# Kernel tuning notes

Hardware: AMD Instinct MI355X
Metric: run time of the kernel (lower is better)

The kernel has to match this reference:

```python
import jax, jax.numpy as jnp
import numpy as np

N_NODES = 10000
N_EDGES = 160000
H = 4            # attention heads
HID = 128        # out_channels == gnn_hidden_dim
C = HID          # per-head channels after .view(-1, H, C) with C = out_channels
HC = H * C       # 512
QD, KD, VD = 19, 16, 18
OUT = 2
SCALE = (HID // H) ** -0.5  # (out_channels // heads) ** -0.5


def _segment_softmax(alpha, idx, n):
    # PyG-style softmax over edges grouped by destination node, per head.
    amax = jax.ops.segment_max(alpha, idx, num_segments=n)          # [n, H]
    ex = jnp.exp(alpha - amax[idx])                                  # [E, H]
    den = jax.ops.segment_sum(ex, idx, num_segments=n)               # [n, H]
    return ex / (den[idx] + 1e-16)


def _gat_layer(qf, kf, vf, pos, src, dst, wq, wk, wv, wo, bo):
    n = qf.shape[0]
    q = (qf @ wq).reshape(n, H, C)
    k = (kf @ wk).reshape(n, H, C)
    v = (vf @ wv).reshape(n, H, C)
    # position-decayed attention: exp(-||pos_i - pos_j||), c_decay = 1.0
    dist = jnp.linalg.norm(pos[dst] - pos[src], axis=-1)             # [E]
    pos_weight = jnp.exp(-dist)
    alpha = (q[dst] * k[src]).sum(-1) * SCALE * pos_weight[:, None]  # [E, H]
    alpha = _segment_softmax(alpha, dst, n)
    out = jax.ops.segment_sum(v[src] * alpha[..., None], dst, num_segments=n)  # [n, H, C]
    return out.reshape(n, HC) @ wo + bo                              # concat heads -> lin_out


def setup_inputs() -> dict:
    key = jax.random.key(0)
    ks = jax.random.split(key, 16)

    def w(k, shape):  # xavier-uniform-ish scale
        return jax.random.normal(k, shape, jnp.float32) * np.float32(np.sqrt(2.0 / (shape[0] + shape[1])))

    obs = jax.random.normal(ks[0], (N_NODES, 37), jnp.float32)
    edge_index = jax.random.randint(ks[1], (2, N_EDGES), 0, N_NODES, jnp.int32)
    return dict(
        obs=obs, edge_index=edge_index,
        wq0=w(ks[2], (QD, HC)), wk0=w(ks[3], (KD, HC)), wv0=w(ks[4], (VD, HC)),
        wo0=w(ks[5], (HC, HID)), bo0=jnp.zeros((HID,), jnp.float32),
        wq1=w(ks[6], (HID, HC)), wk1=w(ks[7], (HID, HC)), wv1=w(ks[8], (HID, HC)),
        wo1=w(ks[9], (HC, HID)), bo1=jnp.zeros((HID,), jnp.float32),
        w1=w(ks[10], (HID, 256)), b1=jnp.zeros((256,), jnp.float32),
        w2=w(ks[11], (256, 256)), b2=jnp.zeros((256,), jnp.float32),
        w3=w(ks[12], (256, OUT)), b3=jnp.zeros((OUT,), jnp.float32),
    )


def reference(obs, edge_index, wq0, wk0, wv0, wo0, bo0, wq1, wk1, wv1, wo1, bo1, w1, b1, w2, b2, w3, b3):
    pos = obs[:, :2]
    # query: agent-self slices 0:12 plus tail slices 30:37 -> 19 dims
    qf = jnp.concatenate([obs[:, :12], obs[:, 30:37]], axis=-1)
    # key: neighbor_block 12:24 + obstacle_block 26:30 -> 16 dims
    kf = jnp.concatenate([obs[:, 12:24], obs[:, 26:30]], axis=-1)
    # value: neighbor_block + neighbor_progress + obstacle_block = 12:30 -> 18 dims
    vf = obs[:, 12:30]
    src, dst = edge_index[0], edge_index[1]
    h = _gat_layer(qf, kf, vf, pos, src, dst, wq0, wk0, wv0, wo0, bo0)
    h = _gat_layer(h, h, h, pos, src, dst, wq1, wk1, wv1, wo1, bo1)
    h = jax.nn.relu(h @ w1 + b1)
    h = jax.nn.relu(h @ w2 + b2)
    return h @ w3 + b3
```

## Files before the change

### kernel.cpp

```cpp
#include <hip/hip_runtime.h>
#include <math.h>

#define NN 10000
#define NE 160000
#define CAP 64
#define SCALE_F 0.17677669529663687f
#define LOG2E_F 1.4426950408889634f

typedef _Float16 f16x8 __attribute__((ext_vector_type(8)));
typedef _Float16 f16x2 __attribute__((ext_vector_type(2)));
typedef float f32x4 __attribute__((ext_vector_type(4)));

#if defined(__has_builtin)
#if __has_builtin(__builtin_amdgcn_global_load_lds)
#define HAS_GLL 1
#endif
#if __has_builtin(__builtin_amdgcn_fdot2)
#define HAS_FDOT2 1
#endif
#endif

struct __align__(8) Edge { int s; float pw; };

__device__ __forceinline__ float dot8_f16(f16x8 a, f16x8 b, float acc) {
#ifdef HAS_FDOT2
#pragma unroll
  for (int e = 0; e < 4; ++e) {
    f16x2 aa = {a[2 * e], a[2 * e + 1]};
    f16x2 bb = {b[2 * e], b[2 * e + 1]};
    acc = __builtin_amdgcn_fdot2(aa, bb, acc, false);
  }
#else
#pragma unroll
  for (int e = 0; e < 8; ++e) acc += (float)a[e] * (float)b[e];
#endif
  return acc;
}

__global__ __launch_bounds__(256) void scatter_kernel(const int* __restrict__ src, const int* __restrict__ dst,
                                                      const float* __restrict__ obs, int* __restrict__ counts,
                                                      Edge* __restrict__ edges) {
  int e = blockIdx.x * 256 + threadIdx.x;
  if (e >= NE) return;
  int s = src[e], d = dst[e];
  int p = atomicAdd(&counts[d], 1);
  float dx = obs[d * 37 + 0] - obs[s * 37 + 0];
  float dy = obs[d * 37 + 1] - obs[s * 37 + 1];
  Edge ee;
  ee.s = s;
  ee.pw = SCALE_F * LOG2E_F * __expf(-sqrtf(dx * dx + dy * dy));
  edges[d * CAP + p] = ee;
}

__global__ __launch_bounds__(256) void prep_kernel(const float* __restrict__ wq0, const float* __restrict__ wk0,
                                                   const float* __restrict__ wv0,
                                                   const float* __restrict__ wo0, const float* __restrict__ wq1,
                                                   const float* __restrict__ wk1, const float* __restrict__ wv1,
                                                   const float* __restrict__ wo1, const float* __restrict__ w1,
                                                   const float* __restrict__ w2, _Float16* __restrict__ dst,
                                                   const float* __restrict__ obs, _Float16* __restrict__ A0,
                                                   int* __restrict__ counts, const float* __restrict__ b3,
                                                   float* __restrict__ outg) {
  int t = blockIdx.x * 256 + threadIdx.x;
  if (t >= 524288) {
    int tp = t - 524288;
    if (tp < NN * 64) {
      int n = tp >> 6, k = tp & 63;
      const float* o = obs + n * 37;
      float x = 0.f;
      if (k < 12) x = o[k];
      else if (k < 19) x = o[30 + k - 12];
      else if (k < 31) x = o[12 + k - 19];
      else if (k < 35) x = o[26 + k - 31];
      else if (k < 53) x = o[12 + k - 35];
      A0[tp] = (_Float16)x;
      return;
    }
    int tz = tp - NN * 64;
    if (tz < NN) { counts[tz] = 0; return; }
    int to = tz - NN;
    if (to < 2 * NN) outg[to] = b3[to & 1];
    return;
  }
  if (t < 98304) {
    int c = t >> 6, k = t & 63;
    float x = 0.f;
    if (c < 512) { if (k < 19) x = wq0[k * 512 + c]; }
    else if (c < 1024) { if (k >= 19 && k < 35) x = wk0[(k - 19) * 512 + (c - 512)]; }
    else { if (k >= 35 && k < 53) x = wv0[(k - 35) * 512 + (c - 1024)]; }
    dst[t] = (_Float16)x;
    return;
  }
  int t1 = t - 98304;
  if (t1 < 196608) {
    int c = t1 >> 7, k = t1 & 127;
    float x;
    if (c < 512) x = wq1[k * 512 + c];
    else if (c < 1024) x = wk1[k * 512 + (c - 512)];
    else x = wv1[k * 512 + (c - 1024)];
    dst[98304 + t1] = (_Float16)x;
    return;
  }
  int t2 = t1 - 196608;
  if (t2 < 65536) { int n = t2 >> 9, k = t2 & 511; dst[294912 + t2] = (_Float16)wo0[k * 128 + n]; return; }
  int t3 = t2 - 65536;
  if (t3 < 65536) { int n = t3 >> 9, k = t3 & 511; dst[360448 + t3] = (_Float16)wo1[k * 128 + n]; return; }
  int t4 = t3 - 65536;
  if (t4 < 32768) { int n = t4 >> 7, k = t4 & 127; dst[425984 + t4] = (_Float16)w1[k * 256 + n]; return; }
  int t5 = t4 - 32768;
  if (t5 < 65536) { int n = t5 >> 8, k = t5 & 255; dst[458752 + t5] = (_Float16)w2[k * 256 + n]; }
}

__global__ __launch_bounds__(256) void gat_kernel(const _Float16* __restrict__ qh, const _Float16* __restrict__ KV,
                                                  const int* __restrict__ counts, const Edge* __restrict__ edges,
                                                  _Float16* __restrict__ attH) {
  int wave = threadIdx.x >> 6, lane = threadIdx.x & 63;
  int grp = lane >> 4, l15 = lane & 15;
  int r = blockIdx.x & 7;
  int c = blockIdx.x >> 3;
  int head = r & 3;
  int chunk = c * 2 + (r >> 2);
  int n = chunk * 4 + wave;
  const _Float16* kvbase = KV + (size_t)head * NN * 256 + l15 * 8;
  f16x8 qv = *(const f16x8*)(qh + (size_t)head * NN * 128 + n * 128 + l15 * 8);
  int cnt = counts[n];
  const Edge* eb = edges + (size_t)n * CAP;
  float den = 0.f;
  float o[8] = {};
  for (int j = grp; j < cnt; j += 8) {
    int jB = j + 4;
    bool actB = jB < cnt;
    int iB = actB ? jB : j;
    Edge eA = eb[j];
    Edge eB = eb[iB];
    const _Float16* pA = kvbase + (size_t)eA.s * 256;
    const _Float16* pB = kvbase + (size_t)eB.s * 256;
    f16x8 kA = *(const f16x8*)pA;
    f16x8 kB = *(const f16x8*)pB;
    f16x8 vA = *(const f16x8*)(pA + 128);
    f16x8 vB = *(const f16x8*)(pB + 128);
    float dA = dot8_f16(qv, kA, 0.f);
    float dB = dot8_f16(qv, kB, 0.f);
    dA += __shfl_xor(dA, 1); dB += __shfl_xor(dB, 1);
    dA += __shfl_xor(dA, 2); dB += __shfl_xor(dB, 2);
    dA += __shfl_xor(dA, 4); dB += __shfl_xor(dB, 4);
    dA += __shfl_xor(dA, 8); dB += __shfl_xor(dB, 8);
    float wA = exp2f(fminf(dA * eA.pw, 80.f));
    float wB = actB ? exp2f(fminf(dB * eB.pw, 80.f)) : 0.f;
    den += wA + wB;
#pragma unroll
    for (int e = 0; e < 8; ++e)
      o[e] += wA * (float)vA[e] + wB * (float)vB[e];
  }
#pragma unroll
  for (int off = 16; off <= 32; off <<= 1) {
    den += __shfl_xor(den, off);
#pragma unroll
    for (int e = 0; e < 8; ++e) o[e] += __shfl_xor(o[e], off);
  }
  if (grp == 0) {
    float inv = 1.f / (den + 1e-16f);
    f16x8 rr;
#pragma unroll
    for (int e = 0; e < 8; ++e) rr[e] = (_Float16)(o[e] * inv);
    *(f16x8*)(attH + (size_t)head * NN * 128 + n * 128 + l15 * 8) = rr;
  }
}

template <int BM, int BIAS, int RELU, int SPLIT, int FUSE3, int SEGA, int PIN>
__global__ __launch_bounds__(256) void gemm_mfma(const _Float16* __restrict__ A, const _Float16* __restrict__ BT,
                                                 const float* __restrict__ bias, _Float16* __restrict__ C,
                                                 _Float16* __restrict__ KV, const float* __restrict__ w3g,
                                                 float* __restrict__ outg, int M, int N, int K) {
  constexpr int ACH = BM / 32;
  constexpr int WR = BM / 2;
  constexpr int RF = WR / 16;
  __shared__ _Float16 As[2][BM * 64];
  __shared__ _Float16 Bs[2][64 * 64];
  int tid = threadIdx.x;
  int wave = tid >> 6, lane = tid & 63;
  int l15 = lane & 15, lq = lane >> 4;
  int wr = (wave >> 1) * WR, wc = (wave & 1) * 32;
  int bx, by;
  if (PIN) {
    int xcd = blockIdx.x & 7, slot = blockIdx.x >> 3;
    int hh = xcd & 3, half = xcd >> 2;
    int i = half * 237 + slot;
    int bg = i / 79;
    bx = i - bg * 79;
    by = (bg < 2) ? (2 * hh + bg) : (bg < 4) ? (8 + 2 * hh + (bg - 2)) : (16 + 2 * hh + (bg - 4));
  } else {
    bx = blockIdx.x;
    by = blockIdx.y;
  }
  int m0 = bx * BM, n0 = by * 64;
  f32x4 acc[RF][2] = {};
  int sw = (l15 & 7) << 4;
  int nt = K >> 6;

  auto stage = [&](int buf, int k0) {
#pragma unroll
    for (int i = 0; i < ACH; ++i) {
      int P = (wave * ACH + i) * 1024 + lane * 16;
      int row = P >> 7;
      int cl = (P & 127) ^ ((row & 7) << 4);
      int gr = m0 + row;
      if (gr > M - 1) gr = M - 1;
      const _Float16* g;
      if (SEGA)
        g = A + (size_t)(k0 >> 7) * (NN * 128) + (size_t)gr * 128 + (k0 & 64) + (cl >> 1);
      else
        g = A + (size_t)gr * K + k0 + (cl >> 1);
#ifdef HAS_GLL
      __builtin_amdgcn_global_load_lds((const __attribute__((address_space(1))) void*)g,
                                       (__attribute__((address_space(3))) void*)((char*)As[buf] + (wave * ACH + i) * 1024),
                                       16, 0, 0);
#else
      uint4 tv = *(const uint4*)g;
      *(uint4*)((char*)As[buf] + P) = tv;
#endif
    }
#pragma unroll
    for (int i = 0; i < 2; ++i) {
      int P = (wave * 2 + i) * 1024 + lane * 16;
      int row = P >> 7;
      int cl = (P & 127) ^ ((row & 7) << 4);
      const _Float16* g = BT + (size_t)(n0 + row) * K + k0 + (cl >> 1);
#ifdef HAS_GLL
      __builtin_amdgcn_global_load_lds((const __attribute__((address_space(1))) void*)g,
                                       (__attribute__((address_space(3))) void*)((char*)Bs[buf] + (wave * 2 + i) * 1024),
                                       16, 0, 0);
#else
      uint4 tv = *(const uint4*)g;
      *(uint4*)((char*)Bs[buf] + P) = tv;
#endif
    }
  };

  stage(0, 0);
  __syncthreads();
  for (int t = 0; t < nt; ++t) {
    int cur = t & 1;
    if (t + 1 < nt) stage(cur ^ 1, (t + 1) << 6);
    const char* pa = (const char*)As[cur];
    const char* pb = (const char*)Bs[cur];
#pragma unroll
    for (int ks = 0; ks < 2; ++ks) {
      int cc = ((ks * 32 + lq * 8) << 1) ^ sw;
      f16x8 b0 = *(const f16x8*)(pb + (wc + 0 + l15) * 128 + cc);
      f16x8 b1 = *(const f16x8*)(pb + (wc + 16 + l15) * 128 + cc);
#pragma unroll
      for (int ri = 0; ri < RF; ++ri) {
        f16x8 a0 = *(const f16x8*)(pa + (wr + ri * 16 + l15) * 128 + cc);
        acc[ri][0] = __builtin_amdgcn_mfma_f32_16x16x32_f16(a0, b0, acc[ri][0], 0, 0, 0);
        acc[ri][1] = __builtin_amdgcn_mfma_f32_16x16x32_f16(a0, b1, acc[ri][1], 0, 0, 0);
      }
    }
    __syncthreads();
  }
#pragma unroll
  for (int ri = 0; ri < RF; ++ri) {
    int gr0 = m0 + wr + ri * 16 + lq * 4;
    float p0[4], p1[4];
#pragma unroll
    for (int jj = 0; jj < 4; ++jj) { p0[jj] = 0.f; p1[jj] = 0.f; }
#pragma unroll
    for (int ci = 0; ci < 2; ++ci) {
      int gc = n0 + wc + ci * 16 + l15;
      float bb = 0.f;
      if (BIAS) bb = bias[gc];
      float w30 = 0.f, w31 = 0.f;
      if (FUSE3) { w30 = w3g[gc * 2 + 0]; w31 = w3g[gc * 2 + 1]; }
#pragma unroll
      for (int jj = 0; jj < 4; ++jj) {
        int gr = gr0 + jj;
        float x = acc[ri][ci][jj] + bb;
        if (RELU) x = fmaxf(x, 0.f);
        if (FUSE3) {
          p0[jj] += x * w30;
          p1[jj] += x * w31;
        } else if (gr < M) {
          _Float16 val = (_Float16)x;
          if (SPLIT) {
            if (gc < 512) {
              int hh = gc >> 7, ch = gc & 127;
              C[((size_t)hh * NN + gr) * 128 + ch] = val;
            } else if (gc < 1024) {
              int hh = (gc - 512) >> 7, ch = (gc - 512) & 127;
              KV[((size_t)hh * NN + gr) * 256 + ch] = val;
            } else {
              int hh = (gc - 1024) >> 7, ch = (gc - 1024) & 127;
              KV[((size_t)hh * NN + gr) * 256 + 128 + ch] = val;
            }
          } else {
            C[(size_t)gr * N + gc] = val;
          }
        }
      }
    }
    if (FUSE3) {
#pragma unroll
      for (int jj = 0; jj < 4; ++jj) {
#pragma unroll
        for (int off = 1; off <= 8; off <<= 1) {
          p0[jj] += __shfl_xor(p0[jj], off);
          p1[jj] += __shfl_xor(p1[jj], off);
        }
        int gr = gr0 + jj;
        if (l15 == 0 && gr < M) {
          atomicAdd(&outg[gr * 2 + 0], p0[jj]);
          atomicAdd(&outg[gr * 2 + 1], p1[jj]);
        }
      }
    }
  }
}

extern "C" void kernel_launch(void* const* d_in, const int* in_sizes, int n_in,
                              void* d_out, int out_size, void* d_ws, size_t ws_size,
                              hipStream_t stream) {
  const float* obs = (const float*)d_in[0];
  const int* eidx = (const int*)d_in[1];
  const float* wq0 = (const float*)d_in[2];
  const float* wk0 = (const float*)d_in[3];
  const float* wv0 = (const float*)d_in[4];
  const float* wo0 = (const float*)d_in[5];
  const float* bo0 = (const float*)d_in[6];
  const float* wq1 = (const float*)d_in[7];
  const float* wk1 = (const float*)d_in[8];
  const float* wv1 = (const float*)d_in[9];
  const float* wo1 = (const float*)d_in[10];
  const float* bo1 = (const float*)d_in[11];
  const float* w1 = (const float*)d_in[12];
  const float* b1 = (const float*)d_in[13];
  const float* w2 = (const float*)d_in[14];
  const float* b2 = (const float*)d_in[15];
  const float* w3 = (const float*)d_in[16];
  const float* b3 = (const float*)d_in[17];
  float* outp = (float*)d_out;

  char* wsb = (char*)d_ws;
  _Float16* qh = (_Float16*)(wsb + 0);
  _Float16* KVB = (_Float16*)(wsb + 10240000);
  _Float16* attH = (_Float16*)(wsb + 30720000);
  _Float16* h = (_Float16*)(wsb + 40960000);
  _Float16* A0 = (_Float16*)(wsb + 43520000);
  _Float16* wT = (_Float16*)(wsb + 44800000);
  int* counts = (int*)(wsb + 45848576);
  Edge* edges = (Edge*)(wsb + 45888576);
  _Float16* m1 = attH;

  _Float16* w0T = wT + 0;
  _Float16* wqkv1T = wT + 98304;
  _Float16* wo0T = wT + 294912;
  _Float16* wo1T = wT + 360448;
  _Float16* w1T = wT + 425984;
  _Float16* w2T = wT + 458752;

  const int* e_src = eidx;
  const int* e_dst = eidx + NE;

  prep_kernel<<<4666, 256, 0, stream>>>(wq0, wk0, wv0, wo0, wq1, wk1, wv1, wo1, w1, w2, wT, obs, A0,
                                        counts, b3, outp);
  scatter_kernel<<<(NE + 255) / 256, 256, 0, stream>>>(e_src, e_dst, obs, counts, edges);

  gemm_mfma<128, 0, 0, 1, 0, 0, 1><<<1896, 256, 0, stream>>>(A0, w0T, nullptr, qh, KVB, nullptr, nullptr, NN, 1536, 64);
  gat_kernel<<<10000, 256, 0, stream>>>(qh, KVB, counts, edges, attH);
  gemm_mfma<64, 1, 0, 0, 0, 1, 0><<<dim3(157, 2), 256, 0, stream>>>(attH, wo0T, bo0, h, nullptr, nullptr, nullptr, NN, 128, 512);

  gemm_mfma<128, 0, 0, 1, 0, 0, 1><<<1896, 256, 0, stream>>>(h, wqkv1T, nullptr, qh, KVB, nullptr, nullptr, NN, 1536, 128);
  gat_kernel<<<10000, 256, 0, stream>>>(qh, KVB, counts, edges, attH);
  gemm_mfma<64, 1, 0, 0, 0, 1, 0><<<dim3(157, 2), 256, 0, stream>>>(attH, wo1T, bo1, h, nullptr, nullptr, nullptr, NN, 128, 512);

  gemm_mfma<64, 1, 1, 0, 0, 0, 0><<<dim3(157, 4), 256, 0, stream>>>(h, w1T, b1, m1, nullptr, nullptr, nullptr, NN, 256, 128);
  gemm_mfma<64, 1, 1, 0, 1, 0, 0><<<dim3(157, 4), 256, 0, stream>>>(m1, w2T, b2, nullptr, nullptr, w3, outp, NN, 256, 256);
}
```

Before: 152.9 us.

## Split GAT into separate weight and aggregation kernels with distinct K/V buffers

The fused GAT kernel is split in two. The first kernel computes the attention logits from K gathers and writes the exponentiated weights to a per-head float buffer. The second re-reads those weights and gathers V to do the weighted aggregation. The QKV GEMM now writes K and V to separate [head, node, 128] arrays instead of an interleaved 256-wide layout, so each pass gathers only 128 halves per row, which is meant to cut the per-kernel gather footprint and improve cache hits. In exchange it adds two extra kernel launches per forward, a write and read of the weight buffer, and a second pass over the edge list.

```diff
diff --git a/kernel.cpp b/kernel.cpp
--- a/kernel.cpp
+++ b/kernel.cpp
@@ -111,9 +111,9 @@
   if (t5 < 65536) { int n = t5 >> 8, k = t5 & 255; dst[458752 + t5] = (_Float16)w2[k * 256 + n]; }
 }
 
-__global__ __launch_bounds__(256) void gat_kernel(const _Float16* __restrict__ qh, const _Float16* __restrict__ KV,
-                                                  const int* __restrict__ counts, const Edge* __restrict__ edges,
-                                                  _Float16* __restrict__ attH) {
+__global__ __launch_bounds__(256) void gatw_kernel(const _Float16* __restrict__ qh, const _Float16* __restrict__ Kh,
+                                                   const int* __restrict__ counts, const Edge* __restrict__ edges,
+                                                   float* __restrict__ wbuf) {
   int wave = threadIdx.x >> 6, lane = threadIdx.x & 63;
   int grp = lane >> 4, l15 = lane & 15;
   int r = blockIdx.x & 7;
@@ -121,24 +121,19 @@
   int head = r & 3;
   int chunk = c * 2 + (r >> 2);
   int n = chunk * 4 + wave;
-  const _Float16* kvbase = KV + (size_t)head * NN * 256 + l15 * 8;
+  const _Float16* kbase = Kh + (size_t)head * NN * 128 + l15 * 8;
   f16x8 qv = *(const f16x8*)(qh + (size_t)head * NN * 128 + n * 128 + l15 * 8);
   int cnt = counts[n];
   const Edge* eb = edges + (size_t)n * CAP;
-  float den = 0.f;
-  float o[8] = {};
+  float* wrow = wbuf + (size_t)head * NN * CAP + (size_t)n * CAP;
   for (int j = grp; j < cnt; j += 8) {
     int jB = j + 4;
     bool actB = jB < cnt;
     int iB = actB ? jB : j;
     Edge eA = eb[j];
     Edge eB = eb[iB];
-    const _Float16* pA = kvbase + (size_t)eA.s * 256;
-    const _Float16* pB = kvbase + (size_t)eB.s * 256;
-    f16x8 kA = *(const f16x8*)pA;
-    f16x8 kB = *(const f16x8*)pB;
-    f16x8 vA = *(const f16x8*)(pA + 128);
-    f16x8 vB = *(const f16x8*)(pB + 128);
+    f16x8 kA = *(const f16x8*)(kbase + (size_t)eA.s * 128);
+    f16x8 kB = *(const f16x8*)(kbase + (size_t)eB.s * 128);
     float dA = dot8_f16(qv, kA, 0.f);
     float dB = dot8_f16(qv, kB, 0.f);
     dA += __shfl_xor(dA, 1); dB += __shfl_xor(dB, 1);
@@ -146,7 +141,40 @@
     dA += __shfl_xor(dA, 4); dB += __shfl_xor(dB, 4);
     dA += __shfl_xor(dA, 8); dB += __shfl_xor(dB, 8);
     float wA = exp2f(fminf(dA * eA.pw, 80.f));
-    float wB = actB ? exp2f(fminf(dB * eB.pw, 80.f)) : 0.f;
+    float wB = exp2f(fminf(dB * eB.pw, 80.f));
+    if (l15 == 0) {
+      wrow[j] = wA;
+      if (actB) wrow[jB] = wB;
+    }
+  }
+}
+
+__global__ __launch_bounds__(256) void gata_kernel(const _Float16* __restrict__ Vh, const int* __restrict__ counts,
+                                                   const Edge* __restrict__ edges, const float* __restrict__ wbuf,
+                                                   _Float16* __restrict__ attH) {
+  int wave = threadIdx.x >> 6, lane = threadIdx.x & 63;
+  int grp = lane >> 4, l15 = lane & 15;
+  int r = blockIdx.x & 7;
+  int c = blockIdx.x >> 3;
+  int head = r & 3;
+  int chunk = c * 2 + (r >> 2);
+  int n = chunk * 4 + wave;
+  const _Float16* vbase = Vh + (size_t)head * NN * 128 + l15 * 8;
+  int cnt = counts[n];
+  const Edge* eb = edges + (size_t)n * CAP;
+  const float* wrow = wbuf + (size_t)head * NN * CAP + (size_t)n * CAP;
+  float den = 0.f;
+  float o[8] = {};
+  for (int j = grp; j < cnt; j += 8) {
+    int jB = j + 4;
+    bool actB = jB < cnt;
+    int iB = actB ? jB : j;
+    int sA = eb[j].s;
+    int sB = eb[iB].s;
+    float wA = wrow[j];
+    float wB = actB ? wrow[jB] : 0.f;
+    f16x8 vA = *(const f16x8*)(vbase + (size_t)sA * 128);
+    f16x8 vB = *(const f16x8*)(vbase + (size_t)sB * 128);
     den += wA + wB;
 #pragma unroll
     for (int e = 0; e < 8; ++e)
@@ -170,8 +198,9 @@
 template <int BM, int BIAS, int RELU, int SPLIT, int FUSE3, int SEGA, int PIN>
 __global__ __launch_bounds__(256) void gemm_mfma(const _Float16* __restrict__ A, const _Float16* __restrict__ BT,
                                                  const float* __restrict__ bias, _Float16* __restrict__ C,
-                                                 _Float16* __restrict__ KV, const float* __restrict__ w3g,
-                                                 float* __restrict__ outg, int M, int N, int K) {
+                                                 _Float16* __restrict__ Kh, _Float16* __restrict__ Vh,
+                                                 const float* __restrict__ w3g, float* __restrict__ outg,
+                                                 int M, int N, int K) {
   constexpr int ACH = BM / 32;
   constexpr int WR = BM / 2;
   constexpr int RF = WR / 16;
@@ -282,16 +311,13 @@
         } else if (gr < M) {
           _Float16 val = (_Float16)x;
           if (SPLIT) {
-            if (gc < 512) {
-              int hh = gc >> 7, ch = gc & 127;
-              C[((size_t)hh * NN + gr) * 128 + ch] = val;
-            } else if (gc < 1024) {
-              int hh = (gc - 512) >> 7, ch = (gc - 512) & 127;
-              KV[((size_t)hh * NN + gr) * 256 + ch] = val;
-            } else {
-              int hh = (gc - 1024) >> 7, ch = (gc - 1024) & 127;
-              KV[((size_t)hh * NN + gr) * 256 + 128 + ch] = val;
-            }
+            _Float16* dstp;
+            int g2;
+            if (gc < 512) { dstp = C; g2 = gc; }
+            else if (gc < 1024) { dstp = Kh; g2 = gc - 512; }
+            else { dstp = Vh; g2 = gc - 1024; }
+            int hh = g2 >> 7, ch = g2 & 127;
+            dstp[((size_t)hh * NN + gr) * 128 + ch] = val;
           } else {
             C[(size_t)gr * N + gc] = val;
           }
@@ -341,13 +367,15 @@
 
   char* wsb = (char*)d_ws;
   _Float16* qh = (_Float16*)(wsb + 0);
-  _Float16* KVB = (_Float16*)(wsb + 10240000);
+  _Float16* KhB = (_Float16*)(wsb + 10240000);
+  _Float16* VhB = (_Float16*)(wsb + 20480000);
   _Float16* attH = (_Float16*)(wsb + 30720000);
   _Float16* h = (_Float16*)(wsb + 40960000);
   _Float16* A0 = (_Float16*)(wsb + 43520000);
   _Float16* wT = (_Float16*)(wsb + 44800000);
   int* counts = (int*)(wsb + 45848576);
   Edge* edges = (Edge*)(wsb + 45888576);
+  float* wbuf = (float*)(wsb + 51008576);
   _Float16* m1 = attH;
 
   _Float16* w0T = wT + 0;
@@ -364,14 +392,16 @@
                                         counts, b3, outp);
   scatter_kernel<<<(NE + 255) / 256, 256, 0, stream>>>(e_src, e_dst, obs, counts, edges);
 
-  gemm_mfma<128, 0, 0, 1, 0, 0, 1><<<1896, 256, 0, stream>>>(A0, w0T, nullptr, qh, KVB, nullptr, nullptr, NN, 1536, 64);
-  gat_kernel<<<10000, 256, 0, stream>>>(qh, KVB, counts, edges, attH);
-  gemm_mfma<64, 1, 0, 0, 0, 1, 0><<<dim3(157, 2), 256, 0, stream>>>(attH, wo0T, bo0, h, nullptr, nullptr, nullptr, NN, 128, 512);
-
-  gemm_mfma<128, 0, 0, 1, 0, 0, 1><<<1896, 256, 0, stream>>>(h, wqkv1T, nullptr, qh, KVB, nullptr, nullptr, NN, 1536, 128);
-  gat_kernel<<<10000, 256, 0, stream>>>(qh, KVB, counts, edges, attH);
-  gemm_mfma<64, 1, 0, 0, 0, 1, 0><<<dim3(157, 2), 256, 0, stream>>>(attH, wo1T, bo1, h, nullptr, nullptr, nullptr, NN, 128, 512);
-
-  gemm_mfma<64, 1, 1, 0, 0, 0, 0><<<dim3(157, 4), 256, 0, stream>>>(h, w1T, b1, m1, nullptr, nullptr, nullptr, NN, 256, 128);
-  gemm_mfma<64, 1, 1, 0, 1, 0, 0><<<dim3(157, 4), 256, 0, stream>>>(m1, w2T, b2, nullptr, nullptr, w3, outp, NN, 256, 256);
-}
+  gemm_mfma<128, 0, 0, 1, 0, 0, 1><<<1896, 256, 0, stream>>>(A0, w0T, nullptr, qh, KhB, VhB, nullptr, nullptr, NN, 1536, 64);
+  gatw_kernel<<<10000, 256, 0, stream>>>(qh, KhB, counts, edges, wbuf);
+  gata_kernel<<<10000, 256, 0, stream>>>(VhB, counts, edges, wbuf, attH);
+  gemm_mfma<64, 1, 0, 0, 0, 1, 0><<<dim3(157, 2), 256, 0, stream>>>(attH, wo0T, bo0, h, nullptr, nullptr, nullptr, nullptr, NN, 128, 512);
+
+  gemm_mfma<128, 0, 0, 1, 0, 0, 1><<<1896, 256, 0, stream>>>(h, wqkv1T, nullptr, qh, KhB, VhB, nullptr, nullptr, NN, 1536, 128);
+  gatw_kernel<<<10000, 256, 0, stream>>>(qh, KhB, counts, edges, wbuf);
+  gata_kernel<<<10000, 256, 0, stream>>>(VhB, counts, edges, wbuf, attH);
+  gemm_mfma<64, 1, 0, 0, 0, 1, 0><<<dim3(157, 2), 256, 0, stream>>>(attH, wo1T, bo1, h, nullptr, nullptr, nullptr, nullptr, NN, 128, 512);
+
+  gemm_mfma<64, 1, 1, 0, 0, 0, 0><<<dim3(157, 4), 256, 0, stream>>>(h, w1T, b1, m1, nullptr, nullptr, nullptr, nullptr, NN, 256, 128);
+  gemm_mfma<64, 1, 1, 0, 1, 0, 0><<<dim3(157, 4), 256, 0, stream>>>(m1, w2T, b2, nullptr, nullptr, nullptr, w3, outp, NN, 256, 256);
+}
```

Result: slower. 185.1 us (+21.1%).
